# Optimization experiments

Measured on AMD Instinct MI355X. Metric: run time of the kernel, lower is better.

The kernel has to match this reference:

```python
import jax, jax.numpy as jnp
import numpy as np

LAMBDA_SOFTMAX = 9.0
EPS = 1e-8


def _l2norm(x, axis):
    # matches torch l2norm: x / (sqrt(sum(x^2)+eps) + eps)
    n = jnp.sqrt(jnp.sum(x * x, axis=axis, keepdims=True) + EPS) + EPS
    return x / n


def setup_inputs() -> dict:
    key = jax.random.key(0)
    k1, k2, k3, k4 = jax.random.split(key, 4)
    n_img, n_cap, n_reg, n_words, d = 128, 128, 36, 48, 1024
    return {
        "img_emb": jax.random.normal(k1, (n_img, n_reg, d), jnp.float32),
        "img_mean": jax.random.normal(k2, (n_img, d), jnp.float32),
        "cap_emb": jax.random.normal(k3, (n_cap, n_words, d), jnp.float32),
        "cap_mean": jax.random.normal(k4, (n_cap, d), jnp.float32),
    }


def reference(img_emb, img_mean, cap_emb, cap_mean):
    # img_emb: [I, R, D]; cap_emb: [C, W, D]
    n_reg = img_emb.shape[1]
    n_words = cap_emb.shape[1]
    # global similarities g[c, i]
    g = cap_mean @ img_mean.T
    # raw dot products S[c, i, r, w] = img_emb[i, r] . cap_emb[c, w]
    S = jnp.einsum('ird,cwd->cirw', img_emb, cap_emb)

    # ---- t2i branch: query=cap (w), context=img (r) ----
    # original attn [i, r, w]: leaky -> l2norm over w -> softmax over r
    a = jax.nn.leaky_relu(S, 0.1)
    a = _l2norm(a, axis=3)
    a = jax.nn.softmax(LAMBDA_SOFTMAX * a, axis=2)
    ra = g[:, :, None, None] * a
    ra = ra / jnp.sum(ra, axis=2, keepdims=True)  # renormalize over source (r)
    # t2i_sim[c, i] = mean_w sum_r ra * S  (since weightedContext.cap = ra contracted with S)
    t2i = jnp.einsum('cirw,cirw->ci', ra, S) / n_words

    # ---- i2t branch: query=img (r), context=cap (w) ----
    # original attn [i, w, r]: leaky -> l2norm over r -> softmax over w
    b = jax.nn.leaky_relu(S, 0.1)
    b = _l2norm(b, axis=2)
    b = jax.nn.softmax(LAMBDA_SOFTMAX * b, axis=3)
    rb = g[:, :, None, None] * b
    rb = rb / jnp.sum(rb, axis=3, keepdims=True)  # renormalize over source (w)
    i2t = jnp.einsum('cirw,cirw->ci', rb, S) / n_reg

    # original returns [n_image, n_caption] (columns appended per caption)
    return (t2i + i2t).T
```

## Files before the change

kernel.cpp:

```cpp
#include <hip/hip_runtime.h>
#include <hip/hip_bf16.h>


#define EPSF 1e-8f
#define LAMF 9.0f

constexpr int IN = 128, CN = 128, RN = 36, WN = 48, DN = 1024;
constexpr size_t NIMG = (size_t)IN * RN * DN;

using short8 = __attribute__((ext_vector_type(8))) short;
using f32x4  = __attribute__((ext_vector_type(4))) float;

__device__ __forceinline__ float leaky(float x) { return x > 0.f ? x : 0.1f * x; }

__device__ __forceinline__ unsigned short f2bf(float f) {
    unsigned int b = __float_as_uint(f);
    b += 0x7FFFu + ((b >> 16) & 1u);
    return (unsigned short)(b >> 16);
}

__device__ __forceinline__ void gld_lds16(const unsigned short* g, void* l) {
    __builtin_amdgcn_global_load_lds(
        (const __attribute__((address_space(1))) unsigned int*)g,
        (__attribute__((address_space(3))) unsigned int*)l,
        16, 0, 0);
}

__global__ void cvt_bf16(const float* __restrict__ in, unsigned short* __restrict__ out, int n4) {
    int idx = blockIdx.x * blockDim.x + threadIdx.x;
    if (idx >= n4) return;
    float4 v = ((const float4*)in)[idx];
    ushort4 o;
    o.x = f2bf(v.x); o.y = f2bf(v.y); o.z = f2bf(v.z); o.w = f2bf(v.w);
    ((ushort4*)out)[idx] = o;
}

__global__ __launch_bounds__(512, 4) void scan_mfma(
    const unsigned short* __restrict__ wsb,
    float* __restrict__ out)
{
    __shared__ __align__(16) unsigned char smem[61824];
    float (*sS)[RN][WN + 1] = (float (*)[RN][WN + 1])smem;
    float* sncol = (float*)(smem + 56448);
    float* snrow = (float*)(smem + 57984);
    float* scw   = (float*)(smem + 59136);
    float* scr   = (float*)(smem + 60672);

    const int t    = threadIdx.x;
    const int lane = t & 63;
    const int wid  = t >> 6;
    const int lr   = lane & 15;
    const int lg   = lane >> 4;
    const int wi   = wid >> 1;
    const int wc   = wid & 1;

    const int bi = blockIdx.x;
    const int bc = blockIdx.y;

    size_t soff[3];
#pragma unroll
    for (int j = 0; j < 3; ++j) {
        int G = (wid + 8 * j) * 64 + lane;
        int row = G >> 2, g = G & 3;
        if (row < 192) {
            int ii = row / 48, rin = row % 48;
            int rsrc = (rin < RN) ? rin : rin - 12;
            int sg = g ^ ((row >> 1) & 3);
            soff[j] = ((size_t)(bi * 4 + ii) * RN + rsrc) * DN + sg * 8;
        } else {
            int crow = row - 192;
            int ci = crow / 48, rin = crow % 48;
            int sg = g ^ ((crow >> 1) & 3);
            soff[j] = NIMG + ((size_t)(bc * 4 + ci) * WN + rin) * DN + sg * 8;
        }
    }

    const int glo = ((lg ^ ((lr >> 1) & 3)) << 4);

    f32x4 acc[3][6];
#pragma unroll
    for (int rt = 0; rt < 3; ++rt)
#pragma unroll
        for (int ct = 0; ct < 6; ++ct) acc[rt][ct] = (f32x4)(0.f);

    auto stage = [&](int bsel, int d0) {
        char* bufp = (char*)smem + bsel * 24576;
#pragma unroll
        for (int j = 0; j < 3; ++j)
            gld_lds16(wsb + soff[j] + d0, bufp + (wid + 8 * j) * 1024);
    };

    stage(0, 0);
    __syncthreads();

    for (int ch = 0; ch < 32; ++ch) {
        if (ch < 31) stage((ch & 1) ^ 1, (ch + 1) * 32);

        const char* bufp = (const char*)smem + (ch & 1) * 24576;
        const char* ap = bufp + (wi * 48 + lr) * 64 + glo;
        short8 a0 = *(const short8*)(ap);
        short8 a1 = *(const short8*)(ap + 1024);
        short8 a2 = *(const short8*)(ap + 2048);
        const char* bp = bufp + 12288 + (wc * 96 + lr) * 64 + glo;
        short8 b[6];
#pragma unroll
        for (int ct = 0; ct < 6; ++ct) b[ct] = *(const short8*)(bp + ct * 1024);

        __builtin_amdgcn_s_setprio(1);
#pragma unroll
        for (int ct = 0; ct < 6; ++ct) {
            acc[0][ct] = __builtin_amdgcn_mfma_f32_16x16x32_bf16(a0, b[ct], acc[0][ct], 0, 0, 0);
            acc[1][ct] = __builtin_amdgcn_mfma_f32_16x16x32_bf16(a1, b[ct], acc[1][ct], 0, 0, 0);
            acc[2][ct] = __builtin_amdgcn_mfma_f32_16x16x32_bf16(a2, b[ct], acc[2][ct], 0, 0, 0);
        }
        __builtin_amdgcn_s_setprio(0);
        __syncthreads();
    }

#pragma unroll
    for (int round = 0; round < 2; ++round) {
        if ((wi >> 1) == round) {
            const int ltb = (wi & 1) * 4 + wc * 2;
#pragma unroll
            for (int rt = 0; rt < 3; ++rt)
#pragma unroll
                for (int ct = 0; ct < 6; ++ct) {
                    int lt = ltb + ct / 3;
                    int col = (ct % 3) * 16 + lr;
#pragma unroll
                    for (int r = 0; r < 4; ++r) {
                        int row = rt * 16 + lg * 4 + r;
                        if (row < RN) sS[lt][row][col] = acc[rt][ct][r];
                    }
                }
        }
        if (round == 1 && t < 8) {
            float s1 = 0.f, s2 = 0.f;
            for (int w = 0; w < WN; ++w) s1 += scw[t * WN + w];
            for (int r = 0; r < RN; ++r) s2 += scr[t * RN + r];
            int i = bi * 4 + (t >> 2), c = bc * 4 + (t & 3);
            out[(size_t)i * CN + c] = s1 / (float)WN + s2 / (float)RN;
        }
        __syncthreads();

        if (t < 8 * WN) {
            int tile = t / WN, w = t % WN;
            float ss = 0.f;
            for (int r = 0; r < RN; ++r) { float l = leaky(sS[tile][r][w]); ss = fmaf(l, l, ss); }
            sncol[t] = LAMF / (sqrtf(ss + EPSF) + EPSF);
        }
        if (t < 8 * RN) {
            int tile = t / RN, r = t % RN;
            float ss = 0.f;
            for (int w = 0; w < WN; ++w) { float l = leaky(sS[tile][r][w]); ss = fmaf(l, l, ss); }
            snrow[t] = LAMF / (sqrtf(ss + EPSF) + EPSF);
        }
        __syncthreads();

        if (t < 8 * RN) {
            int tile = t / RN, r = t % RN;
            const float* Sr = sS[tile][r];
            const float* ic = sncol + tile * WN;
            float se = 0.f, sw = 0.f;
            for (int w = 0; w < WN; ++w) {
                float s = Sr[w];
                float e = __expf(leaky(s) * ic[w]);
                se += e;
                sw = fmaf(e, s, sw);
            }
            scr[t] = sw / se;
        }
        if (t < 8 * WN) {
            int tile = t / WN, w = t % WN;
            const float* ir = snrow + tile * RN;
            float se = 0.f, sw = 0.f;
            for (int r = 0; r < RN; ++r) {
                float s = sS[tile][r][w];
                float e = __expf(leaky(s) * ir[r]);
                se += e;
                sw = fmaf(e, s, sw);
            }
            scw[t] = sw / se;
        }
        __syncthreads();

        if (round == 1 && t < 8) {
            float s1 = 0.f, s2 = 0.f;
            for (int w = 0; w < WN; ++w) s1 += scw[t * WN + w];
            for (int r = 0; r < RN; ++r) s2 += scr[t * RN + r];
            int i = bi * 4 + 2 + (t >> 2), c = bc * 4 + (t & 3);
            out[(size_t)i * CN + c] = s1 / (float)WN + s2 / (float)RN;
        }
    }
}

__global__ __launch_bounds__(256, 4) void scan_fused(
    const float* __restrict__ img_emb, const float* __restrict__ cap_emb,
    float* __restrict__ out)
{
    __shared__ float s_img[48][68];
    __shared__ float s_cap[48][68];
    __shared__ float s_S[RN][WN + 1];
    __shared__ float s_nrow[RN];
    __shared__ float s_ncol[WN];
    __shared__ float s_cw[WN];
    __shared__ float s_cr[RN];

    const int t = threadIdx.x;
    const int c = blockIdx.x & (CN - 1);
    const int i = blockIdx.x >> 7;
    const float* imgB = img_emb + (size_t)i * RN * DN;
    const float* capB = cap_emb + (size_t)c * WN * DN;
    const int ty = t >> 4, tx = t & 15;

    float4 acc[3][3];
#pragma unroll
    for (int a = 0; a < 3; ++a)
#pragma unroll
        for (int b = 0; b < 3; ++b) acc[a][b] = make_float4(0.f, 0.f, 0.f, 0.f);

    for (int d0 = 0; d0 < DN; d0 += 64) {
#pragma unroll
        for (int p = 0; p < 3; ++p) {
            int idx = t + p * 256, row = idx >> 4, col = (idx & 15) << 2;
            float4 v = make_float4(0.f, 0.f, 0.f, 0.f);
            if (row < RN) v = *(const float4*)(imgB + row * DN + d0 + col);
            *(float4*)&s_img[row][col] = v;
        }
#pragma unroll
        for (int p = 0; p < 3; ++p) {
            int idx = t + p * 256, row = idx >> 4, col = (idx & 15) << 2;
            *(float4*)&s_cap[row][col] = *(const float4*)(capB + row * DN + d0 + col);
        }
        __syncthreads();
        for (int d = 0; d < 64; d += 4) {
            float4 a0 = *(float4*)&s_img[ty][d], a1 = *(float4*)&s_img[ty + 16][d], a2 = *(float4*)&s_img[ty + 32][d];
            float4 b0 = *(float4*)&s_cap[tx][d], b1 = *(float4*)&s_cap[tx + 16][d], b2 = *(float4*)&s_cap[tx + 32][d];
#define F4(ac, aa, bb) ac.x=fmaf(aa.x,bb.x,ac.x); ac.y=fmaf(aa.y,bb.y,ac.y); ac.z=fmaf(aa.z,bb.z,ac.z); ac.w=fmaf(aa.w,bb.w,ac.w)
            F4(acc[0][0],a0,b0); F4(acc[0][1],a0,b1); F4(acc[0][2],a0,b2);
            F4(acc[1][0],a1,b0); F4(acc[1][1],a1,b1); F4(acc[1][2],a1,b2);
            F4(acc[2][0],a2,b0); F4(acc[2][1],a2,b1); F4(acc[2][2],a2,b2);
#undef F4
        }
        __syncthreads();
    }
#pragma unroll
    for (int a = 0; a < 3; ++a) {
        int r = ty + 16 * a;
        if (r < RN)
#pragma unroll
            for (int b = 0; b < 3; ++b) {
                float4 v = acc[a][b];
                s_S[r][tx + 16 * b] = (v.x + v.y) + (v.z + v.w);
            }
    }
    __syncthreads();
    if (t < RN) {
        float ss = 0.f;
        for (int w = 0; w < WN; ++w) { float l = leaky(s_S[t][w]); ss = fmaf(l, l, ss); }
        s_nrow[t] = sqrtf(ss + EPSF) + EPSF;
    } else if (t >= 64 && t < 64 + WN) {
        int w = t - 64; float ss = 0.f;
        for (int r = 0; r < RN; ++r) { float l = leaky(s_S[r][w]); ss = fmaf(l, l, ss); }
        s_ncol[w] = sqrtf(ss + EPSF) + EPSF;
    }
    __syncthreads();
    if (t < RN) {
        float se = 0.f, sw = 0.f;
        for (int w = 0; w < WN; ++w) {
            float e = __expf(LAMF * leaky(s_S[t][w]) / s_ncol[w]);
            se += e; sw = fmaf(e, s_S[t][w], sw);
        }
        s_cr[t] = sw / se;
    } else if (t >= 64 && t < 64 + WN) {
        int w = t - 64;
        float se = 0.f, sw = 0.f;
        for (int r = 0; r < RN; ++r) {
            float e = __expf(LAMF * leaky(s_S[r][w]) / s_nrow[r]);
            se += e; sw = fmaf(e, s_S[r][w], sw);
        }
        s_cw[w] = sw / se;
    }
    __syncthreads();
    if (t == 0) {
        float t2i = 0.f, i2t = 0.f;
        for (int w = 0; w < WN; ++w) t2i += s_cw[w];
        for (int r = 0; r < RN; ++r) i2t += s_cr[r];
        out[(size_t)i * CN + c] = t2i / (float)WN + i2t / (float)RN;
    }
}

extern "C" void kernel_launch(void* const* d_in, const int* in_sizes, int n_in,
                              void* d_out, int out_size, void* d_ws, size_t ws_size,
                              hipStream_t stream) {
    const float* img = (const float*)d_in[0];
    const float* cap = (const float*)d_in[2];
    float* out = (float*)d_out;

    const size_t n_img = NIMG;
    const size_t n_cap = (size_t)CN * WN * DN;
    const size_t need  = (n_img + n_cap) * 2;

    if (ws_size >= need) {
        unsigned short* imgh = (unsigned short*)d_ws;
        unsigned short* caph = imgh + n_img;
        int n4i = (int)(n_img / 4), n4c = (int)(n_cap / 4);
        hipLaunchKernelGGL(cvt_bf16, dim3((n4i + 255) / 256), dim3(256), 0, stream, img, imgh, n4i);
        hipLaunchKernelGGL(cvt_bf16, dim3((n4c + 255) / 256), dim3(256), 0, stream, cap, caph, n4c);
        hipLaunchKernelGGL(scan_mfma, dim3(IN / 4, CN / 4), dim3(512), 0, stream, imgh, out);
    } else {
        hipLaunchKernelGGL(scan_fused, dim3(IN * CN), dim3(256), 0, stream, img, cap, out);
    }
}
```

Before: 104.7 us.

## Remove padded image rows and remap MFMA tiles to 4 waves

Packs the 4 images' 36 regions contiguously (144 rows instead of 192 padded rows), so the MFMA tile covers 9x16 rows with no wasted padding compute or loads. Each of 4 waves now owns one caption's 48 words and all 144 image rows (9x3 MFMAs per chunk, A fragments loaded per row tile). Block size drops from 512 to 256 threads and LDS per buffer shrinks, and the epilogue is processed in 4 rounds, one per image, instead of 2. The trade-off is fewer waves per block, more accumulator registers per thread, and more serialized epilogue rounds.

Result: no change. 105.5 us (+0.8%).

```diff
diff --git a/kernel.cpp b/kernel.cpp
--- a/kernel.cpp
+++ b/kernel.cpp
@@ -7,6 +7,12 @@
 
 constexpr int IN = 128, CN = 128, RN = 36, WN = 48, DN = 1024;
 constexpr size_t NIMG = (size_t)IN * RN * DN;
+
+constexpr int AROWS = 4 * RN;
+constexpr int BROWS = 4 * WN;
+constexpr int TROWS = AROWS + BROWS;
+constexpr int BUFB  = TROWS * 64;
+constexpr int NGRAN = TROWS * 4;
 
 using short8 = __attribute__((ext_vector_type(8))) short;
 using f32x4  = __attribute__((ext_vector_type(4))) float;
@@ -35,59 +41,55 @@
     ((ushort4*)out)[idx] = o;
 }
 
-__global__ __launch_bounds__(512, 4) void scan_mfma(
+__global__ __launch_bounds__(256, 3) void scan_mfma(
     const unsigned short* __restrict__ wsb,
     float* __restrict__ out)
 {
-    __shared__ __align__(16) unsigned char smem[61824];
+    __shared__ __align__(16) unsigned char smem[2 * BUFB];
     float (*sS)[RN][WN + 1] = (float (*)[RN][WN + 1])smem;
-    float* sncol = (float*)(smem + 56448);
-    float* snrow = (float*)(smem + 57984);
-    float* scw   = (float*)(smem + 59136);
-    float* scr   = (float*)(smem + 60672);
+    float* sncol = (float*)(smem + 28224);
+    float* snrow = (float*)(smem + 28992);
+    float* scw   = (float*)(smem + 29568);
+    float* scr   = (float*)(smem + 30336);
 
     const int t    = threadIdx.x;
     const int lane = t & 63;
     const int wid  = t >> 6;
     const int lr   = lane & 15;
     const int lg   = lane >> 4;
-    const int wi   = wid >> 1;
-    const int wc   = wid & 1;
 
     const int bi = blockIdx.x;
     const int bc = blockIdx.y;
 
-    size_t soff[3];
-#pragma unroll
-    for (int j = 0; j < 3; ++j) {
-        int G = (wid + 8 * j) * 64 + lane;
-        int row = G >> 2, g = G & 3;
-        if (row < 192) {
-            int ii = row / 48, rin = row % 48;
-            int rsrc = (rin < RN) ? rin : rin - 12;
-            int sg = g ^ ((row >> 1) & 3);
-            soff[j] = ((size_t)(bi * 4 + ii) * RN + rsrc) * DN + sg * 8;
-        } else {
-            int crow = row - 192;
-            int ci = crow / 48, rin = crow % 48;
-            int sg = g ^ ((crow >> 1) & 3);
-            soff[j] = NIMG + ((size_t)(bc * 4 + ci) * WN + rin) * DN + sg * 8;
-        }
+    unsigned int soff[6];
+#pragma unroll
+    for (int j = 0; j < 6; ++j) {
+        int g = (j < 5) ? (j * 256 + t) : (1280 + t);
+        int row = g >> 2, cg = g & 3;
+        int sg = cg ^ ((row >> 1) & 3);
+        unsigned int off;
+        if (row < AROWS)
+            off = (unsigned int)((bi * AROWS + row) << 10) + sg * 8;
+        else
+            off = (unsigned int)NIMG + (unsigned int)((bc * BROWS + (row - AROWS)) << 10) + sg * 8;
+        soff[j] = off;
     }
 
     const int glo = ((lg ^ ((lr >> 1) & 3)) << 4);
 
-    f32x4 acc[3][6];
-#pragma unroll
-    for (int rt = 0; rt < 3; ++rt)
-#pragma unroll
-        for (int ct = 0; ct < 6; ++ct) acc[rt][ct] = (f32x4)(0.f);
+    f32x4 acc[9][3];
+#pragma unroll
+    for (int rt = 0; rt < 9; ++rt)
+#pragma unroll
+        for (int ct = 0; ct < 3; ++ct) acc[rt][ct] = (f32x4)(0.f);
 
     auto stage = [&](int bsel, int d0) {
-        char* bufp = (char*)smem + bsel * 24576;
-#pragma unroll
-        for (int j = 0; j < 3; ++j)
-            gld_lds16(wsb + soff[j] + d0, bufp + (wid + 8 * j) * 1024);
+        char* bufp = (char*)smem + bsel * BUFB;
+#pragma unroll
+        for (int j = 0; j < 5; ++j)
+            gld_lds16(wsb + soff[j] + d0, bufp + j * 4096 + wid * 1024);
+        if (t < 64)
+            gld_lds16(wsb + soff[5] + d0, bufp + 20480);
     };
 
     stage(0, 0);
@@ -96,70 +98,65 @@
     for (int ch = 0; ch < 32; ++ch) {
         if (ch < 31) stage((ch & 1) ^ 1, (ch + 1) * 32);
 
-        const char* bufp = (const char*)smem + (ch & 1) * 24576;
-        const char* ap = bufp + (wi * 48 + lr) * 64 + glo;
-        short8 a0 = *(const short8*)(ap);
-        short8 a1 = *(const short8*)(ap + 1024);
-        short8 a2 = *(const short8*)(ap + 2048);
-        const char* bp = bufp + 12288 + (wc * 96 + lr) * 64 + glo;
-        short8 b[6];
-#pragma unroll
-        for (int ct = 0; ct < 6; ++ct) b[ct] = *(const short8*)(bp + ct * 1024);
+        const char* bufp = (const char*)smem + (ch & 1) * BUFB;
+        const char* ap = bufp + lr * 64 + glo;
+        const char* bp = bufp + (AROWS + wid * WN + lr) * 64 + glo;
+        short8 b0 = *(const short8*)(bp);
+        short8 b1 = *(const short8*)(bp + 1024);
+        short8 b2 = *(const short8*)(bp + 2048);
 
         __builtin_amdgcn_s_setprio(1);
 #pragma unroll
-        for (int ct = 0; ct < 6; ++ct) {
-            acc[0][ct] = __builtin_amdgcn_mfma_f32_16x16x32_bf16(a0, b[ct], acc[0][ct], 0, 0, 0);
-            acc[1][ct] = __builtin_amdgcn_mfma_f32_16x16x32_bf16(a1, b[ct], acc[1][ct], 0, 0, 0);
-            acc[2][ct] = __builtin_amdgcn_mfma_f32_16x16x32_bf16(a2, b[ct], acc[2][ct], 0, 0, 0);
+        for (int rt = 0; rt < 9; ++rt) {
+            short8 a = *(const short8*)(ap + rt * 1024);
+            acc[rt][0] = __builtin_amdgcn_mfma_f32_16x16x32_bf16(a, b0, acc[rt][0], 0, 0, 0);
+            acc[rt][1] = __builtin_amdgcn_mfma_f32_16x16x32_bf16(a, b1, acc[rt][1], 0, 0, 0);
+            acc[rt][2] = __builtin_amdgcn_mfma_f32_16x16x32_bf16(a, b2, acc[rt][2], 0, 0, 0);
         }
         __builtin_amdgcn_s_setprio(0);
         __syncthreads();
     }
 
 #pragma unroll
-    for (int round = 0; round < 2; ++round) {
-        if ((wi >> 1) == round) {
-            const int ltb = (wi & 1) * 4 + wc * 2;
-#pragma unroll
-            for (int rt = 0; rt < 3; ++rt)
-#pragma unroll
-                for (int ct = 0; ct < 6; ++ct) {
-                    int lt = ltb + ct / 3;
-                    int col = (ct % 3) * 16 + lr;
-#pragma unroll
-                    for (int r = 0; r < 4; ++r) {
-                        int row = rt * 16 + lg * 4 + r;
-                        if (row < RN) sS[lt][row][col] = acc[rt][ct][r];
-                    }
-                }
-        }
-        if (round == 1 && t < 8) {
+    for (int r = 0; r < 4; ++r) {
+        if (r > 0 && t < 4) {
             float s1 = 0.f, s2 = 0.f;
             for (int w = 0; w < WN; ++w) s1 += scw[t * WN + w];
-            for (int r = 0; r < RN; ++r) s2 += scr[t * RN + r];
-            int i = bi * 4 + (t >> 2), c = bc * 4 + (t & 3);
-            out[(size_t)i * CN + c] = s1 / (float)WN + s2 / (float)RN;
-        }
-        __syncthreads();
-
-        if (t < 8 * WN) {
+            for (int rr = 0; rr < RN; ++rr) s2 += scr[t * RN + rr];
+            out[(size_t)(bi * 4 + (r - 1)) * CN + (bc * 4 + t)] = s1 / (float)WN + s2 / (float)RN;
+        }
+#pragma unroll
+        for (int rt = 0; rt < 9; ++rt)
+#pragma unroll
+            for (int reg = 0; reg < 4; ++reg) {
+                int lrow = rt * 16 + lg * 4 + reg;
+                int ii = lrow / 36;
+                if (ii == r) {
+                    int rin = lrow - ii * 36;
+#pragma unroll
+                    for (int ct = 0; ct < 3; ++ct)
+                        sS[wid][rin][ct * 16 + lr] = acc[rt][ct][reg];
+                }
+            }
+        __syncthreads();
+
+        if (t < 4 * WN) {
             int tile = t / WN, w = t % WN;
             float ss = 0.f;
-            for (int r = 0; r < RN; ++r) { float l = leaky(sS[tile][r][w]); ss = fmaf(l, l, ss); }
+            for (int rr = 0; rr < RN; ++rr) { float l = leaky(sS[tile][rr][w]); ss = fmaf(l, l, ss); }
             sncol[t] = LAMF / (sqrtf(ss + EPSF) + EPSF);
         }
-        if (t < 8 * RN) {
-            int tile = t / RN, r = t % RN;
+        if (t < 4 * RN) {
+            int tile = t / RN, rr = t % RN;
             float ss = 0.f;
-            for (int w = 0; w < WN; ++w) { float l = leaky(sS[tile][r][w]); ss = fmaf(l, l, ss); }
+            for (int w = 0; w < WN; ++w) { float l = leaky(sS[tile][rr][w]); ss = fmaf(l, l, ss); }
             snrow[t] = LAMF / (sqrtf(ss + EPSF) + EPSF);
         }
         __syncthreads();
 
-        if (t < 8 * RN) {
-            int tile = t / RN, r = t % RN;
-            const float* Sr = sS[tile][r];
+        if (t < 4 * RN) {
+            int tile = t / RN, rr = t % RN;
+            const float* Sr = sS[tile][rr];
             const float* ic = sncol + tile * WN;
             float se = 0.f, sw = 0.f;
             for (int w = 0; w < WN; ++w) {
@@ -170,27 +167,26 @@
             }
             scr[t] = sw / se;
         }
-        if (t < 8 * WN) {
+        if (t < 4 * WN) {
             int tile = t / WN, w = t % WN;
             const float* ir = snrow + tile * RN;
             float se = 0.f, sw = 0.f;
-            for (int r = 0; r < RN; ++r) {
-                float s = sS[tile][r][w];
-                float e = __expf(leaky(s) * ir[r]);
+            for (int rr = 0; rr < RN; ++rr) {
+                float s = sS[tile][rr][w];
+                float e = __expf(leaky(s) * ir[rr]);
                 se += e;
                 sw = fmaf(e, s, sw);
             }
             scw[t] = sw / se;
         }
         __syncthreads();
-
-        if (round == 1 && t < 8) {
-            float s1 = 0.f, s2 = 0.f;
-            for (int w = 0; w < WN; ++w) s1 += scw[t * WN + w];
-            for (int r = 0; r < RN; ++r) s2 += scr[t * RN + r];
-            int i = bi * 4 + 2 + (t >> 2), c = bc * 4 + (t & 3);
-            out[(size_t)i * CN + c] = s1 / (float)WN + s2 / (float)RN;
-        }
+    }
+
+    if (t < 4) {
+        float s1 = 0.f, s2 = 0.f;
+        for (int w = 0; w < WN; ++w) s1 += scw[t * WN + w];
+        for (int rr = 0; rr < RN; ++rr) s2 += scr[t * RN + rr];
+        out[(size_t)(bi * 4 + 3) * CN + (bc * 4 + t)] = s1 / (float)WN + s2 / (float)RN;
     }
 }
 
@@ -307,7 +303,7 @@
         int n4i = (int)(n_img / 4), n4c = (int)(n_cap / 4);
         hipLaunchKernelGGL(cvt_bf16, dim3((n4i + 255) / 256), dim3(256), 0, stream, img, imgh, n4i);
         hipLaunchKernelGGL(cvt_bf16, dim3((n4c + 255) / 256), dim3(256), 0, stream, cap, caph, n4c);
-        hipLaunchKernelGGL(scan_mfma, dim3(IN / 4, CN / 4), dim3(512), 0, stream, imgh, out);
+        hipLaunchKernelGGL(scan_mfma, dim3(IN / 4, CN / 4), dim3(256), 0, stream, imgh, out);
     } else {
         hipLaunchKernelGGL(scan_fused, dim3(IN * CN), dim3(256), 0, stream, img, cap, out);
     }
```
